# Kernel tuning notes

Hardware: AMD Instinct MI355X
Metric: run time of the kernel (lower is better)

Reference implementation:

```python
import jax, jax.numpy as jnp
import numpy as np

R_CUT = 10.0  # init arg r_cut


def _per_mol(pos, T, eneg, node_attrs, an, q_tot, eidx, hardness, cov_radii):
    # pos [N,3], T [N,E], eneg [N], node_attrs [N,num_el], an [N] int,
    # q_tot scalar, eidx [2,E] int
    N = pos.shape[0]
    E = T.shape[1]
    dtype = pos.dtype
    sqrt_pi = jnp.sqrt(jnp.pi).astype(dtype)
    sqrt_2 = jnp.sqrt(2.0).astype(dtype)
    eye = jnp.eye(N, dtype=dtype)
    # pairwise distances; +eye makes the (masked-out) diagonal sqrt-safe
    diff = pos[:, None, :] - pos[None, :, :]
    d = jnp.sqrt(jnp.sum(diff * diff, axis=-1) + eye)  # [N,N]
    r = cov_radii[an]                                   # [N]
    sigma = r * r
    gamma = jnp.sqrt(sigma[:, None] + sigma[None, :])   # [N,N]
    diag_vals = hardness[jnp.argmax(node_attrs, axis=-1)] + 1.0 / (sqrt_pi * r)
    A = jax.scipy.special.erf(d / (sqrt_2 * gamma)) / d * (1.0 - eye) + jnp.diag(diag_vals)
    # per-edge cutoff diagonal: 1/cos(pi*r/(2*r_cut)) - 1
    e0, e1 = eidx[0], eidx[1]
    edge_d = jnp.sqrt(jnp.sum((pos[e0] - pos[e1]) ** 2, axis=-1))  # [E]
    cut = 1.0 / jnp.cos(jnp.pi * edge_d / (2.0 * R_CUT)) - 1.0
    Ap = T.T @ A @ T + jnp.diag(cut)                    # [E,E]
    # augment with charge-conservation row/col of ones
    ones_col = jnp.ones((E, 1), dtype=dtype)
    ones_row = jnp.ones((1, E + 1), dtype=dtype)
    Aaug = jnp.concatenate([jnp.concatenate([Ap, ones_col], axis=1), ones_row], axis=0)
    b = jnp.concatenate([-(T.T @ eneg), q_tot[None]])   # [E+1]
    x = jnp.linalg.solve(Aaug, b)[:-1]                  # [E] split charges
    return T @ x                                        # [N] atomic partial charges


def setup_inputs() -> dict:
    key = jax.random.key(0)
    B, N, E, NUM_EL, NZ = 256, 64, 512, 10, 119
    ks = jax.random.split(key, 10)
    positions = jax.random.normal(ks[0], (B, N, 3), dtype=jnp.float32)
    T = jax.random.normal(ks[1], (B, N, E), dtype=jnp.float32)
    eneg = jax.random.normal(ks[2], (B, N), dtype=jnp.float32)
    node_attrs = jax.random.normal(ks[3], (B, N, NUM_EL), dtype=jnp.float32)
    total_charge = jax.random.normal(ks[4], (B,), dtype=jnp.float32)
    atomic_numbers = jax.random.randint(ks[5], (B, N), 1, 100)
    e0 = jax.random.randint(ks[6], (B, E), 0, N)
    off = jax.random.randint(ks[7], (B, E), 1, N)
    edge_index = jnp.stack([e0, (e0 + off) % N], axis=1)  # [B,2,E], distinct endpoints
    hardness = jax.random.uniform(ks[8], (NUM_EL,), dtype=jnp.float32)
    cov_radii = 0.3 + 2.2 * jax.random.uniform(ks[9], (NZ,), dtype=jnp.float32)
    p = jnp.zeros((1,), dtype=jnp.float32)  # only used for .device in torch
    return dict(positions=positions, T=T, eneg=eneg, node_attrs=node_attrs,
                total_charge=total_charge, p=p, hardness=hardness,
                cov_radii=cov_radii, atomic_numbers=atomic_numbers,
                edge_index=edge_index)


def reference(positions, T, eneg, node_attrs, total_charge, p, hardness,
              cov_radii, atomic_numbers, edge_index):
    charges = jax.vmap(_per_mol, in_axes=(0, 0, 0, 0, 0, 0, 0, None, None))(
        positions, T, eneg, node_attrs, atomic_numbers, total_charge,
        edge_index, hardness, cov_radii)  # [B,N]
    return charges.reshape(-1)  # concat over molecules, as in the torch loop
```

## Files before the change

### kernel.cpp

```cpp
#include <hip/hip_runtime.h>
#include <math.h>

#define SQRT_PI 1.7724538509055160273
#define SQRT_2  1.4142135623730950488
#define PI_OVER_2RC 0.15707963267948966

typedef double dbl4 __attribute__((ext_vector_type(4)));


__device__ __forceinline__ double bcast64(double v, int lane) {
    union { double d; unsigned int u[2]; } a, r;
    a.d = v;
    r.u[0] = __builtin_amdgcn_readlane(a.u[0], lane);
    r.u[1] = __builtin_amdgcn_readlane(a.u[1], lane);
    return r.d;
}

__device__ __forceinline__ double a_entry(int i, int j, const double* posd,
                                          const double* sig, const double* dg) {
    if (i == j) return dg[i];
    double dx = posd[3*i+0]-posd[3*j+0];
    double dy = posd[3*i+1]-posd[3*j+1];
    double dz = posd[3*i+2]-posd[3*j+2];
    double d  = sqrt(dx*dx+dy*dy+dz*dz);
    double g  = sqrt(sig[i]+sig[j]);
    return erf(d/(SQRT_2*g))/d;
}

__device__ __forceinline__ dbl4 mfma64(int cS, double xv, double yv, dbl4 acc) {
    return cS ? __builtin_amdgcn_mfma_f64_16x16x4f64(yv, xv, acc, 0, 0, 0)
              : __builtin_amdgcn_mfma_f64_16x16x4f64(xv, yv, acc, 0, 0, 0);
}

__global__ __launch_bounds__(64)
void k0_probe(double* __restrict__ fl)
{
    const int l = threadIdx.x;
    const int kl = l >> 4, ml = l & 15;
    const double af1 = (double)(l + 1),  bf1 = (double)(l + 65);
    const double af2 = (double)(1 + ((l*7 + 3) % 61));
    const double bf2 = (double)(2 + ((l*13 + 5) % 53));
    dbl4 c1 = {0.0,0.0,0.0,0.0}, c2 = {0.0,0.0,0.0,0.0};
    c1 = __builtin_amdgcn_mfma_f64_16x16x4f64(af1, bf1, c1, 0, 0, 0);
    c2 = __builtin_amdgcn_mfma_f64_16x16x4f64(af2, bf2, c2, 0, 0, 0);
    int best = -1;
    for (int h = 0; h < 32; ++h) {
        if (best >= 0) break;
        const int cS = h >> 4, cA = (h >> 3) & 1, cB = (h >> 2) & 1, cD = h & 3;
        bool ok = true;
        #pragma unroll
        for (int r = 0; r < 4; ++r) {
            int row, col;
            const int v0 = 4*kl + r, v1 = kl + 4*r;
            if (cD == 0)      { row = v0; col = ml; }
            else if (cD == 1) { row = v1; col = ml; }
            else if (cD == 2) { row = ml; col = v0; }
            else              { row = ml; col = v1; }
            double r1 = 0.0, r2 = 0.0;
            #pragma unroll
            for (int k = 0; k < 4; ++k) {
                const int la = cA ? (row*4 + k) : (row + 16*k);
                const int lb = cB ? (col*4 + k) : (col + 16*k);
                if (cS == 0) {
                    r1 += (double)(la + 1) * (double)(lb + 65);
                    r2 += (double)(1 + ((la*7+3) % 61)) * (double)(2 + ((lb*13+5) % 53));
                } else {
                    r1 += (double)(lb + 1) * (double)(la + 65);
                    r2 += (double)(1 + ((lb*7+3) % 61)) * (double)(2 + ((la*13+5) % 53));
                }
            }
            if (c1[r] != r1 || c2[r] != r2) ok = false;
        }
        if (__ballot(ok) == ~0ull) best = h;
    }
    if (l == 0) {
        fl[0] = (best >= 0) ? 1.0 : 0.0;
        fl[1] = (double)((best >= 0) ? (best >> 4)      : 0);
        fl[2] = (double)((best >= 0) ? ((best >> 3) & 1) : 0);
        fl[3] = (double)((best >= 0) ? ((best >> 2) & 1) : 0);
        fl[4] = (double)((best >= 0) ? (best & 3)        : 0);
    }
}

__global__ __launch_bounds__(1024)
void k_fused(const float* __restrict__ pos, const float* __restrict__ T,
             const int* __restrict__ eidx, const float* __restrict__ nattr,
             const float* __restrict__ eneg, const float* __restrict__ qtot,
             const float* __restrict__ hard, const float* __restrict__ covr,
             const int* __restrict__ an, const double* __restrict__ flq,
             float* __restrict__ outp)
{
    const int m = blockIdx.x, tid = threadIdx.x;
    const int jl = tid & 63;
    const int rg = tid >> 6;
    const int kl = jl >> 4, ml = jl & 15;

    __shared__ double R[2*64*66];
    __shared__ double AB[64*65];
    __shared__ double w_sl[512];
    __shared__ double posd[192], sig_s[64], dg_s[64], eneg_s[64];
    __shared__ double t0a_s[64], t0b_s[64], ga_s[64], gb_s[64];
    __shared__ double ua_s[64], ub_s[64];
    __shared__ double dinv_s[64], dvec_s[64];
    __shared__ double lam_sh, sw_sh;

    double* const Ta = R;
    double* const Tb = R + 64*66;
    double* const SB = R;
    double* const Pm = R + 64*66;

    const int cS = (int)flq[1], cA = (int)flq[2], cB = (int)flq[3], cD = (int)flq[4];
    const int aRow = cA ? (jl >> 2) : ml;
    const int aK   = cA ? (jl & 3)  : kl;
    const int bRow = cB ? (jl >> 2) : ml;
    const int bK   = cB ? (jl & 3)  : kl;
    int drow[4], dcol[4];
    #pragma unroll
    for (int r = 0; r < 4; ++r) {
        const int v0 = 4*kl + r, v1 = kl + 4*r;
        if (cD == 0)      { drow[r] = v0; dcol[r] = ml; }
        else if (cD == 1) { drow[r] = v1; dcol[r] = ml; }
        else if (cD == 2) { drow[r] = ml; dcol[r] = v0; }
        else              { drow[r] = ml; dcol[r] = v1; }
    }

    const float* Tm = T + (size_t)m*64*512;
    const int srow = tid >> 4, sc4 = (tid & 15) * 4;

    float4 v = *(const float4*)&Tm[srow*512 + sc4];

    if (tid < 64) {
        posd[3*tid+0] = (double)pos[(m*64+tid)*3+0];
        posd[3*tid+1] = (double)pos[(m*64+tid)*3+1];
        posd[3*tid+2] = (double)pos[(m*64+tid)*3+2];
        double r = (double)covr[an[m*64+tid]];
        sig_s[tid] = r*r;
        const float* np_ = nattr + (size_t)(m*64+tid)*10;
        float best = np_[0]; int bi = 0;
        #pragma unroll
        for (int k = 1; k < 10; ++k) { float vv = np_[k]; if (vv > best) { best = vv; bi = k; } }
        dg_s[tid] = (double)hard[bi] + 1.0/(SQRT_PI*r);
    } else if (tid < 128) {
        int ll = tid - 64;
        eneg_s[ll] = (double)eneg[m*64 + ll];
    }
    __syncthreads();

    if (tid < 512) {
        const int a0 = eidx[(size_t)m*1024 + tid];
        const int a1 = eidx[(size_t)m*1024 + 512 + tid];
        double dx = posd[3*a0+0]-posd[3*a1+0];
        double dy = posd[3*a0+1]-posd[3*a1+1];
        double dz = posd[3*a0+2]-posd[3*a1+2];
        double d  = sqrt(dx*dx+dy*dy+dz*dz);
        w_sl[tid] = 1.0 / (1.0/cos(PI_OVER_2RC*d) - 1.0);
    }

    int tp, tq, wm;
    switch (rg) {
        case 0:  tp=0; tq=0; wm=0; break;
        case 5:  tp=1; tq=1; wm=0; break;
        case 10: tp=2; tq=2; wm=0; break;
        case 15: tp=3; tq=3; wm=0; break;
        case 1:  tp=1; tq=0; wm=1; break;
        case 2:  tp=1; tq=0; wm=2; break;
        case 3:  tp=2; tq=0; wm=1; break;
        case 4:  tp=2; tq=0; wm=2; break;
        case 6:  tp=2; tq=1; wm=1; break;
        case 7:  tp=2; tq=1; wm=2; break;
        case 8:  tp=3; tq=0; wm=1; break;
        case 9:  tp=3; tq=0; wm=2; break;
        case 11: tp=3; tq=1; wm=1; break;
        case 12: tp=3; tq=1; wm=2; break;
        case 13: tp=3; tq=2; wm=1; break;
        default: tp=3; tq=2; wm=2; break;
    }
    const double* ta_b = &Ta[(size_t)(tp*16 + aRow)*66 + aK];
    const double* tb_b = &Tb[(size_t)(tq*16 + bRow)*66 + bK];
    dbl4 vacc = {0.0, 0.0, 0.0, 0.0};
    double t0b_p = 0.0;
    double areg[4];

    #pragma unroll
    for (int cc = 0; cc < 8; ++cc) {
        __syncthreads();
        const double w0 = w_sl[cc*64 + sc4+0];
        const double w1 = w_sl[cc*64 + sc4+1];
        const double w2 = w_sl[cc*64 + sc4+2];
        const double w3 = w_sl[cc*64 + sc4+3];
        const double d0 = (double)v.x, d1 = (double)v.y;
        const double d2 = (double)v.z, d3 = (double)v.w;
        {
            double2 p0; p0.x = d0; p0.y = d1;
            double2 p1; p1.x = d2; p1.y = d3;
            *(double2*)&Ta[srow*66 + sc4]     = p0;
            *(double2*)&Ta[srow*66 + sc4 + 2] = p1;
            double2 q0; q0.x = w0*d0; q0.y = w1*d1;
            double2 q1; q1.x = w2*d2; q1.y = w3*d3;
            *(double2*)&Tb[srow*66 + sc4]     = q0;
            *(double2*)&Tb[srow*66 + sc4 + 2] = q1;
        }
        t0b_p += d0*w0 + d1*w1 + d2*w2 + d3*w3;
        __syncthreads();
        if (cc < 7) v = *(const float4*)&Tm[srow*512 + (cc+1)*64 + sc4];
        if (cc == 0 && tid >= 128 && tid < 192) {
            const int ll = tid - 128;
            double s = 0.0;
            #pragma unroll
            for (int c = 0; c < 8; ++c) s += w_sl[c*64 + ll];
            #pragma unroll
            for (int off = 32; off > 0; off >>= 1) s += __shfl_down(s, off);
            if (ll == 0) sw_sh = s;
        }
        if (cc < 4) {
            const int i = rg + 16*cc;
            double av = a_entry(i, jl, posd, sig_s, dg_s);
            areg[cc] = av;
            AB[i*65 + jl] = av;
        }
        const bool act = (wm == 0) || (wm == 1 ? ((cc & 1) == 0) : ((cc & 1) == 1));
        if (act) {
            #pragma unroll
            for (int kk = 0; kk < 16; ++kk)
                vacc = mfma64(cS, ta_b[kk*4], tb_b[kk*4], vacc);
        }
    }
    __syncthreads();

    if (wm != 2) {
        #pragma unroll
        for (int r = 0; r < 4; ++r) {
            const int ri = tp*16 + drow[r], cj = tq*16 + dcol[r];
            SB[ri*66 + cj] = vacc[r];
            if (tp != tq) SB[cj*66 + ri] = vacc[r];
        }
    }
    {
        double t = t0b_p;
        t += __shfl_down(t, 8, 16);
        t += __shfl_down(t, 4, 16);
        t += __shfl_down(t, 2, 16);
        t += __shfl_down(t, 1, 16);
        if ((tid & 15) == 0) t0b_s[tid >> 4] = t;
    }
    __syncthreads();
    if (wm == 2) {
        #pragma unroll
        for (int r = 0; r < 4; ++r) {
            const int ri = tp*16 + drow[r], cj = tq*16 + dcol[r];
            const double vv = vacc[r];
            SB[ri*66 + cj] += vv;
            if (tp != tq) SB[cj*66 + ri] += vv;
        }
    }
    __syncthreads();

    {
        const int c16 = tid & 15, row16 = tid >> 4;
        double a = 0.0;
        #pragma unroll
        for (int kk = 0; kk < 4; ++kk)
            a += SB[row16*66 + 4*c16 + kk] * eneg_s[4*c16 + kk];
        a += __shfl_down(a, 8, 16);
        a += __shfl_down(a, 4, 16);
        a += __shfl_down(a, 2, 16);
        a += __shfl_down(a, 1, 16);
        if (c16 == 0) t0a_s[row16] = -a;
    }
    __syncthreads();

    {
        double ra[4], rb[4];
        const double ta = t0a_s[jl], tb = t0b_s[jl];
        #pragma unroll
        for (int p = 0; p < 4; ++p) { ra[p] = areg[p]*ta; rb[p] = areg[p]*tb; }
        #pragma unroll
        for (int off = 32; off > 0; off >>= 1) {
            #pragma unroll
            for (int p = 0; p < 4; ++p) {
                ra[p] += __shfl_down(ra[p], off);
                rb[p] += __shfl_down(rb[p], off);
            }
        }
        if (jl == 0) {
            #pragma unroll
            for (int p = 0; p < 4; ++p) { ga_s[rg+16*p] = ra[p]; gb_s[rg+16*p] = rb[p]; }
        }
    }
    __syncthreads();

    const int ti = rg >> 2, tj = rg & 3;
    {
        const double* xb = &AB[(size_t)(ti*16 + aRow)*65 + aK];
        const double* yb = &SB[(size_t)bK*66 + tj*16 + bRow];
        dbl4 pacc = {0.0, 0.0, 0.0, 0.0};
        #pragma unroll
        for (int kk = 0; kk < 16; ++kk)
            pacc = mfma64(cS, xb[kk*4], yb[kk*264], pacc);
        #pragma unroll
        for (int r = 0; r < 4; ++r)
            Pm[(ti*16 + drow[r])*66 + tj*16 + dcol[r]] = pacc[r];
    }
    __syncthreads();

    {
        dbl4 macc;
        #pragma unroll
        for (int r = 0; r < 4; ++r)
            macc[r] = AB[(ti*16 + drow[r])*65 + tj*16 + dcol[r]];
        const double* xb = &Pm[(size_t)(ti*16 + aRow)*66 + aK];
        const double* yb = &AB[(size_t)bK*65 + tj*16 + bRow];
        #pragma unroll
        for (int kk = 0; kk < 16; ++kk)
            macc = mfma64(cS, xb[kk*4], yb[kk*260], macc);
        __syncthreads();
        #pragma unroll
        for (int r = 0; r < 4; ++r)
            AB[(ti*16 + drow[r])*65 + tj*16 + dcol[r]] = macc[r];
    }
    __syncthreads();

    for (int pb = 0; pb < 4; ++pb) {
        const int kb = pb*16;
        if (tid < 64) {
            const int i = tid;
            double pr[16];
            #pragma unroll
            for (int c = 0; c < 16; ++c) pr[c] = AB[i*65 + kb + c];
            #pragma unroll
            for (int c = 0; c < 16; ++c) {
                const int k = kb + c;
                const double Dk = bcast64(pr[c], k);
                const double di = 1.0 / Dk;
                if (i == k) { dinv_s[k] = di; dvec_s[k] = Dk; }
                const double lik = pr[c] * di;
                #pragma unroll
                for (int j = c+1; j < 16; ++j) {
                    const double mkj = bcast64(pr[j], k);
                    if (i > k) pr[j] -= lik * mkj;
                }
                if (i > k) pr[c] = lik;
            }
            #pragma unroll
            for (int c = 0; c < 16; ++c) AB[i*65 + kb + c] = pr[c];
        }
        __syncthreads();
        const int lim = kb + 16;
        if (lim < 64) {
            double tacc[4] = {0.0, 0.0, 0.0, 0.0};
            #pragma unroll 4
            for (int c = 0; c < 16; ++c) {
                double lbv = AB[jl*65 + kb + c] * dvec_s[kb + c];
                #pragma unroll
                for (int p = 0; p < 4; ++p)
                    tacc[p] += AB[(rg+16*p)*65 + kb + c] * lbv;
            }
            if (jl >= lim) {
                #pragma unroll
                for (int p = 0; p < 4; ++p) {
                    int i = rg + 16*p;
                    if (i >= lim) AB[i*65 + jl] -= tacc[p];
                }
            }
        }
        __syncthreads();
    }

    if (tid < 128) {
        const int i = jl;
        double h = (rg == 0) ? ga_s[i] : gb_s[i];
        #pragma unroll
        for (int j = 0; j < 63; ++j) {
            double x = bcast64(h, j);
            double lij = (i > j) ? AB[i*65+j] : 0.0;
            h -= lij*x;
        }
        h *= dinv_s[i];
        #pragma unroll
        for (int j = 63; j > 0; --j) {
            double x = bcast64(h, j);
            double lji = (i < j) ? AB[j*65+i] : 0.0;
            h -= lji*x;
        }
        if (rg == 0) ua_s[i] = h; else ub_s[i] = h;
    }
    __syncthreads();

    if (tid < 64) {
        const double ua = ua_s[tid], ub = ub_s[tid], gbv = gb_s[tid];
        double d1 = eneg_s[tid]*t0b_s[tid] + ua*gbv;
        double d2 = ub*gbv;
        #pragma unroll
        for (int off = 32; off > 0; off >>= 1) {
            d1 += __shfl_down(d1, off);
            d2 += __shfl_down(d2, off);
        }
        if (tid == 0) {
            double sY = -d1;
            double sZ = sw_sh - d2;
            lam_sh = ((double)qtot[m] - sY) / (1.0 - sZ);
        }
    }
    __syncthreads();
    if (tid < 64)
        outp[m*64 + tid] = (float)(ua_s[tid] - lam_sh*ub_s[tid]);
}

extern "C" void kernel_launch(void* const* d_in, const int* in_sizes, int n_in,
                              void* d_out, int out_size, void* d_ws, size_t ws_size,
                              hipStream_t stream) {
    const float* pos  = (const float*)d_in[0];
    const float* T    = (const float*)d_in[1];
    const float* eneg = (const float*)d_in[2];
    const float* nat  = (const float*)d_in[3];
    const float* qt   = (const float*)d_in[4];
    const float* hard = (const float*)d_in[6];
    const float* covr = (const float*)d_in[7];
    const int*   an   = (const int*)d_in[8];
    const int*   eidx = (const int*)d_in[9];
    float* outp = (float*)d_out;
    (void)n_in; (void)out_size; (void)ws_size;

    const int B = in_sizes[4];
    double* ws = (double*)d_ws;

    k0_probe<<<dim3(1), dim3(64), 0, stream>>>(ws);
    k_fused<<<dim3(B), dim3(1024), 0, stream>>>(pos, T, eidx, nat, eneg, qt,
                                                hard, covr, an, ws, outp);
}
```

Before: 160.3 us.

## Use symmetric sqrt-weighted T factor to compute Gram matrix with single staging buffer

Instead of staging both T and W*T tiles and multiplying them, the kernel scales T columns by sqrt(w) and forms the Gram matrix from one buffer, so each 128-edge chunk fills the space previously used by two 64-edge tiles. This halves the number of chunk iterations and their barriers, and doubles the MFMA work per iteration. It relies on w being non-negative for sqrt, which holds when cos is positive for distances below the cutoff. It also adds a sqrt per edge and a second weight array in shared memory.

```diff
diff --git a/kernel.cpp b/kernel.cpp
--- a/kernel.cpp
+++ b/kernel.cpp
@@ -95,17 +95,17 @@
     const int rg = tid >> 6;
     const int kl = jl >> 4, ml = jl & 15;
 
-    __shared__ double R[2*64*66];
+    __shared__ double R[8448];
     __shared__ double AB[64*65];
     __shared__ double w_sl[512];
+    __shared__ double rw_sl[512];
     __shared__ double posd[192], sig_s[64], dg_s[64], eneg_s[64];
     __shared__ double t0a_s[64], t0b_s[64], ga_s[64], gb_s[64];
     __shared__ double ua_s[64], ub_s[64];
     __shared__ double dinv_s[64], dvec_s[64];
     __shared__ double lam_sh, sw_sh;
 
-    double* const Ta = R;
-    double* const Tb = R + 64*66;
+    double* const Cd = R;
     double* const SB = R;
     double* const Pm = R + 64*66;
 
@@ -127,7 +127,8 @@
     const float* Tm = T + (size_t)m*64*512;
     const int srow = tid >> 4, sc4 = (tid & 15) * 4;
 
-    float4 v = *(const float4*)&Tm[srow*512 + sc4];
+    float4 v0r = *(const float4*)&Tm[srow*512 + sc4];
+    float4 v1r = *(const float4*)&Tm[srow*512 + 64 + sc4];
 
     if (tid < 64) {
         posd[3*tid+0] = (double)pos[(m*64+tid)*3+0];
@@ -153,7 +154,9 @@
         double dy = posd[3*a0+1]-posd[3*a1+1];
         double dz = posd[3*a0+2]-posd[3*a1+2];
         double d  = sqrt(dx*dx+dy*dy+dz*dz);
-        w_sl[tid] = 1.0 / (1.0/cos(PI_OVER_2RC*d) - 1.0);
+        double w  = 1.0 / (1.0/cos(PI_OVER_2RC*d) - 1.0);
+        w_sl[tid]  = w;
+        rw_sl[tid] = sqrt(w);
     }
 
     int tp, tq, wm;
@@ -175,35 +178,37 @@
         case 13: tp=3; tq=2; wm=1; break;
         default: tp=3; tq=2; wm=2; break;
     }
-    const double* ta_b = &Ta[(size_t)(tp*16 + aRow)*66 + aK];
-    const double* tb_b = &Tb[(size_t)(tq*16 + bRow)*66 + bK];
+    const double* ca_b = &Cd[(size_t)(tp*16 + aRow)*130 + aK];
+    const double* cb_b = &Cd[(size_t)(tq*16 + bRow)*130 + bK];
     dbl4 vacc = {0.0, 0.0, 0.0, 0.0};
     double t0b_p = 0.0;
     double areg[4];
 
     #pragma unroll
-    for (int cc = 0; cc < 8; ++cc) {
+    for (int st = 0; st < 4; ++st) {
         __syncthreads();
-        const double w0 = w_sl[cc*64 + sc4+0];
-        const double w1 = w_sl[cc*64 + sc4+1];
-        const double w2 = w_sl[cc*64 + sc4+2];
-        const double w3 = w_sl[cc*64 + sc4+3];
-        const double d0 = (double)v.x, d1 = (double)v.y;
-        const double d2 = (double)v.z, d3 = (double)v.w;
+        const int eA = st*128 + sc4;
+        const int eB = eA + 64;
         {
-            double2 p0; p0.x = d0; p0.y = d1;
-            double2 p1; p1.x = d2; p1.y = d3;
-            *(double2*)&Ta[srow*66 + sc4]     = p0;
-            *(double2*)&Ta[srow*66 + sc4 + 2] = p1;
-            double2 q0; q0.x = w0*d0; q0.y = w1*d1;
-            double2 q1; q1.x = w2*d2; q1.y = w3*d3;
-            *(double2*)&Tb[srow*66 + sc4]     = q0;
-            *(double2*)&Tb[srow*66 + sc4 + 2] = q1;
-        }
-        t0b_p += d0*w0 + d1*w1 + d2*w2 + d3*w3;
+            double2 p0; p0.x = (double)v0r.x * rw_sl[eA+0]; p0.y = (double)v0r.y * rw_sl[eA+1];
+            double2 p1; p1.x = (double)v0r.z * rw_sl[eA+2]; p1.y = (double)v0r.w * rw_sl[eA+3];
+            *(double2*)&Cd[srow*130 + sc4]     = p0;
+            *(double2*)&Cd[srow*130 + sc4 + 2] = p1;
+            double2 q0; q0.x = (double)v1r.x * rw_sl[eB+0]; q0.y = (double)v1r.y * rw_sl[eB+1];
+            double2 q1; q1.x = (double)v1r.z * rw_sl[eB+2]; q1.y = (double)v1r.w * rw_sl[eB+3];
+            *(double2*)&Cd[srow*130 + 64 + sc4]     = q0;
+            *(double2*)&Cd[srow*130 + 64 + sc4 + 2] = q1;
+        }
+        t0b_p += (double)v0r.x*w_sl[eA+0] + (double)v0r.y*w_sl[eA+1]
+               + (double)v0r.z*w_sl[eA+2] + (double)v0r.w*w_sl[eA+3]
+               + (double)v1r.x*w_sl[eB+0] + (double)v1r.y*w_sl[eB+1]
+               + (double)v1r.z*w_sl[eB+2] + (double)v1r.w*w_sl[eB+3];
         __syncthreads();
-        if (cc < 7) v = *(const float4*)&Tm[srow*512 + (cc+1)*64 + sc4];
-        if (cc == 0 && tid >= 128 && tid < 192) {
+        if (st < 3) {
+            v0r = *(const float4*)&Tm[srow*512 + (st+1)*128 + sc4];
+            v1r = *(const float4*)&Tm[srow*512 + (st+1)*128 + 64 + sc4];
+        }
+        if (st == 0 && tid >= 128 && tid < 192) {
             const int ll = tid - 128;
             double s = 0.0;
             #pragma unroll
@@ -212,17 +217,17 @@
             for (int off = 32; off > 0; off >>= 1) s += __shfl_down(s, off);
             if (ll == 0) sw_sh = s;
         }
-        if (cc < 4) {
-            const int i = rg + 16*cc;
+        {
+            const int i = rg + 16*st;
             double av = a_entry(i, jl, posd, sig_s, dg_s);
-            areg[cc] = av;
+            areg[st] = av;
             AB[i*65 + jl] = av;
         }
-        const bool act = (wm == 0) || (wm == 1 ? ((cc & 1) == 0) : ((cc & 1) == 1));
+        const bool act = (wm == 0) || (wm == 1 ? ((st & 1) == 0) : ((st & 1) == 1));
         if (act) {
             #pragma unroll
-            for (int kk = 0; kk < 16; ++kk)
-                vacc = mfma64(cS, ta_b[kk*4], tb_b[kk*4], vacc);
+            for (int kk = 0; kk < 32; ++kk)
+                vacc = mfma64(cS, ca_b[kk*4], cb_b[kk*4], vacc);
         }
     }
     __syncthreads();
```

After: 178.4 us. 1.11x slower.
